# Kernel optimization log

Measured on AMD Instinct MI355X. Metric: run time of the kernel, lower is better.

## Reference

```python
import jax, jax.numpy as jnp
import numpy as np

D = 512      # n_embd
H = 8        # n_head
L = 2        # n_layer (per stack)
T = 2048     # sequence length / block_size
B = 1        # batch
BANDS = (999, 9)  # band_width for [phase, tool] stacks
EPS = 1e-5


def _sinusoidal(n_pos, dim):
    pos = np.arange(n_pos)[:, None].astype(np.float64)
    j = np.arange(dim)[None, :]
    angle = pos / np.power(10000.0, 2 * (j // 2) / dim)
    out = np.zeros((n_pos, dim), np.float32)
    out[:, 0::2] = np.sin(angle[:, 0::2])
    out[:, 1::2] = np.cos(angle[:, 1::2])
    return jnp.asarray(out)


def setup_inputs() -> dict:
    key = jax.random.key(0)
    ks = jax.random.split(key, 8)
    s = 0.02
    rn = lambda k, shp: jax.random.normal(k, shp, jnp.float32) * s
    inp = {
        "x": jax.random.normal(ks[0], (B, T, D), jnp.float32),
        "pos_emb": _sinusoidal(T, D),            # sinusoidal, frozen
        # leading dim 2 = [phase stack, tool stack], then layer dim L
        "ln1_w": jnp.ones((2, L, D)), "ln1_b": jnp.zeros((2, L, D)),
        "ln2_w": jnp.ones((2, L, D)), "ln2_b": jnp.zeros((2, L, D)),
        "Wq": rn(ks[1], (2, L, D, D)), "bq": jnp.zeros((2, L, D)),
        "Wk": rn(ks[2], (2, L, D, D)), "bk": jnp.zeros((2, L, D)),
        "Wv": rn(ks[3], (2, L, D, D)), "bv": jnp.zeros((2, L, D)),
        "Wo": rn(ks[4], (2, L, D, D)), "bo": jnp.zeros((2, L, D)),
        "W1": rn(ks[5], (2, L, D, 2 * D)), "b1": jnp.zeros((2, L, 2 * D)),
        "W2": rn(ks[6], (2, L, 2 * D, D)), "b2": jnp.zeros((2, L, D)),
        "lnf_w": jnp.ones((D,)), "lnf_b": jnp.zeros((D,)),
    }
    return inp


def _ln(x, w, b):
    mu = x.mean(-1, keepdims=True)
    var = ((x - mu) ** 2).mean(-1, keepdims=True)
    return (x - mu) / jnp.sqrt(var + EPS) * w + b


def _attn(x, Wq, bq, Wk, bk, Wv, bv, Wo, bo, bw):
    Bx, Tx, _ = x.shape
    Dh = D // H
    heads = lambda W, b: (x @ W + b).reshape(Bx, Tx, H, Dh).transpose(0, 2, 1, 3)
    q, k, v = heads(Wq, bq), heads(Wk, bk), heads(Wv, bv)
    att = jnp.einsum('bhqd,bhkd->bhqk', q, k) / jnp.sqrt(jnp.float32(Dh))
    i = jnp.arange(Tx)[:, None]
    j = jnp.arange(Tx)[None, :]
    mask = (j <= i) & (j >= i - bw)  # causal band
    att = jnp.where(mask, att, -jnp.inf)
    att = jax.nn.softmax(att, axis=-1)
    y = jnp.einsum('bhqk,bhkd->bhqd', att, v).transpose(0, 2, 1, 3).reshape(Bx, Tx, D)
    return y @ Wo + bo


def reference(x, pos_emb, ln1_w, ln1_b, ln2_w, ln2_b,
              Wq, bq, Wk, bk, Wv, bv, Wo, bo,
              W1, b1, W2, b2, lnf_w, lnf_b):
    Tx = x.shape[1]
    h0 = x + pos_emb[None, :Tx]
    outs = []
    for s in range(2):  # phase stack, tool stack
        bw = BANDS[s]
        h = h0
        for l in range(L):
            h = h + _attn(_ln(h, ln1_w[s, l], ln1_b[s, l]),
                          Wq[s, l], bq[s, l], Wk[s, l], bk[s, l],
                          Wv[s, l], bv[s, l], Wo[s, l], bo[s, l], bw)
            hm = _ln(h, ln2_w[s, l], ln2_b[s, l])
            h = h + (jax.nn.gelu(hm @ W1[s, l] + b1[s, l], approximate=False)
                     @ W2[s, l] + b2[s, l])
        outs.append(_ln(h, lnf_w, lnf_b))
    return (outs[0], outs[1])
```

## Files before the change

### kernel.cpp

```cpp
#include <hip/hip_runtime.h>
#include <stdint.h>

#define T 2048
#define D 512
#define NH 8
#define DH 64
#define L 2

typedef float floatx4 __attribute__((ext_vector_type(4)));
typedef short shortx8 __attribute__((ext_vector_type(8)));
typedef unsigned short u16;
typedef unsigned short u16x4 __attribute__((ext_vector_type(4)));

__device__ __forceinline__ u16 f2bf(float f) {
    union { float f; uint32_t u; } c; c.f = f;
    uint32_t u = c.u;
    u += 0x7fffu + ((u >> 16) & 1u);
    return (u16)(u >> 16);
}

__device__ __forceinline__ float bf2f(u16 v) {
    union { uint32_t u; float f; } c; c.u = ((uint32_t)v) << 16;
    return c.f;
}

__device__ __forceinline__ void load_lds16(const void* g, void* l) {
    __builtin_amdgcn_global_load_lds((const __attribute__((address_space(1))) void*)g,
                                     (__attribute__((address_space(3))) void*)l,
                                     16, 0, 0);
}

struct TransJobs {
    const float* src[6];
    u16* dst[6];
    const float* x;
    const float* pos;
    float* h;
};

__global__ __launch_bounds__(256) void pre_kernel(TransJobs j) {
    __shared__ float tile[32][33];
    int tid = threadIdx.x;
    if (blockIdx.z == 24) {
        int idx = (blockIdx.y * 32 + blockIdx.x) * 256 + tid;
        float4 xv = ((const float4*)j.x)[idx];
        float4 pv = ((const float4*)j.pos)[idx];
        float4 r;
        r.x = xv.x + pv.x; r.y = xv.y + pv.y; r.z = xv.z + pv.z; r.w = xv.w + pv.w;
        ((float4*)j.h)[idx] = r;
        ((float4*)j.h)[idx + (T * D / 4)] = r;
        return;
    }
    int m = blockIdx.z >> 2, slice = blockIdx.z & 3;
    int R = (m == 5) ? 1024 : 512;
    int C = (m == 4) ? 1024 : 512;
    if (blockIdx.x * 32 >= C || blockIdx.y * 32 >= R) return;
    const float* in = j.src[m] + (size_t)slice * R * C;
    u16* out = j.dst[m] + (size_t)slice * R * C;
    int tx = tid & 31, ty = tid >> 5;
    int x = blockIdx.x * 32 + tx;
    int y0 = blockIdx.y * 32;
#pragma unroll
    for (int i = 0; i < 4; i++)
        tile[ty + i * 8][tx] = in[(size_t)(y0 + ty + i * 8) * C + x];
    __syncthreads();
    int ox = y0 + tx;
#pragma unroll
    for (int i = 0; i < 4; i++)
        out[(size_t)(blockIdx.x * 32 + ty + i * 8) * R + ox] = f2bf(tile[tx][ty + i * 8]);
}

__global__ __launch_bounds__(256) void ln_res_kernel(float* __restrict__ h,
                                                     const u16* __restrict__ part,
                                                     const float* __restrict__ w0,
                                                     const float* __restrict__ b0,
                                                     u16* __restrict__ out, int l) {
    int row = blockIdx.x * 4 + (threadIdx.x >> 6);
    int lane = threadIdx.x & 63;
    int s = row >> 11;
    int c0 = lane * 4;
    float* xr = h + (size_t)row * D;
    float4 v0 = *(const float4*)(xr + c0);
    float4 v1 = *(const float4*)(xr + c0 + 256);
    if (part) {
        const u16* p0r = part + (size_t)s * 2 * T * D + (size_t)(row & (T - 1)) * D;
        const u16* p1r = p0r + (size_t)T * D;
        u16x4 a0 = *(const u16x4*)(p0r + c0), a1 = *(const u16x4*)(p0r + c0 + 256);
        u16x4 e0 = *(const u16x4*)(p1r + c0), e1 = *(const u16x4*)(p1r + c0 + 256);
        v0.x += bf2f(a0[0]) + bf2f(e0[0]); v0.y += bf2f(a0[1]) + bf2f(e0[1]);
        v0.z += bf2f(a0[2]) + bf2f(e0[2]); v0.w += bf2f(a0[3]) + bf2f(e0[3]);
        v1.x += bf2f(a1[0]) + bf2f(e1[0]); v1.y += bf2f(a1[1]) + bf2f(e1[1]);
        v1.z += bf2f(a1[2]) + bf2f(e1[2]); v1.w += bf2f(a1[3]) + bf2f(e1[3]);
        *(float4*)(xr + c0) = v0;
        *(float4*)(xr + c0 + 256) = v1;
    }
    float sum = v0.x + v0.y + v0.z + v0.w + v1.x + v1.y + v1.z + v1.w;
    float sq = v0.x*v0.x + v0.y*v0.y + v0.z*v0.z + v0.w*v0.w
             + v1.x*v1.x + v1.y*v1.y + v1.z*v1.z + v1.w*v1.w;
#pragma unroll
    for (int d2 = 1; d2 < 64; d2 <<= 1) { sum += __shfl_xor(sum, d2); sq += __shfl_xor(sq, d2); }
    float mu = sum * (1.0f / D);
    float var = sq * (1.0f / D) - mu * mu;
    float rstd = rsqrtf(var + 1e-5f);
    const float* w = w0 + (size_t)(s * L + l) * D;
    const float* b = b0 + (size_t)(s * L + l) * D;
    u16x4 p0, p1;
#pragma unroll
    for (int jj = 0; jj < 4; jj++) {
        float a = (jj == 0 ? v0.x : jj == 1 ? v0.y : jj == 2 ? v0.z : v0.w);
        p0[jj] = f2bf((a - mu) * rstd * w[c0 + jj] + b[c0 + jj]);
        float c = (jj == 0 ? v1.x : jj == 1 ? v1.y : jj == 2 ? v1.z : v1.w);
        p1[jj] = f2bf((c - mu) * rstd * w[c0 + 256 + jj] + b[c0 + 256 + jj]);
    }
    *(u16x4*)(out + (size_t)row * D + c0) = p0;
    *(u16x4*)(out + (size_t)row * D + c0 + 256) = p1;
}

__global__ __launch_bounds__(256) void lnf_kernel(const float* __restrict__ h,
                                                  const u16* __restrict__ part,
                                                  const float* __restrict__ w,
                                                  const float* __restrict__ b,
                                                  float* __restrict__ out) {
    int row = blockIdx.x * 4 + (threadIdx.x >> 6);
    int lane = threadIdx.x & 63;
    int s = row >> 11;
    int c0 = lane * 4;
    const float* xr = h + (size_t)row * D;
    float4 v0 = *(const float4*)(xr + c0);
    float4 v1 = *(const float4*)(xr + c0 + 256);
    const u16* p0r = part + (size_t)s * 2 * T * D + (size_t)(row & (T - 1)) * D;
    const u16* p1r = p0r + (size_t)T * D;
    u16x4 a0 = *(const u16x4*)(p0r + c0), a1 = *(const u16x4*)(p0r + c0 + 256);
    u16x4 e0 = *(const u16x4*)(p1r + c0), e1 = *(const u16x4*)(p1r + c0 + 256);
    v0.x += bf2f(a0[0]) + bf2f(e0[0]); v0.y += bf2f(a0[1]) + bf2f(e0[1]);
    v0.z += bf2f(a0[2]) + bf2f(e0[2]); v0.w += bf2f(a0[3]) + bf2f(e0[3]);
    v1.x += bf2f(a1[0]) + bf2f(e1[0]); v1.y += bf2f(a1[1]) + bf2f(e1[1]);
    v1.z += bf2f(a1[2]) + bf2f(e1[2]); v1.w += bf2f(a1[3]) + bf2f(e1[3]);
    float sum = v0.x + v0.y + v0.z + v0.w + v1.x + v1.y + v1.z + v1.w;
    float sq = v0.x*v0.x + v0.y*v0.y + v0.z*v0.z + v0.w*v0.w
             + v1.x*v1.x + v1.y*v1.y + v1.z*v1.z + v1.w*v1.w;
#pragma unroll
    for (int d2 = 1; d2 < 64; d2 <<= 1) { sum += __shfl_xor(sum, d2); sq += __shfl_xor(sq, d2); }
    float mu = sum * (1.0f / D);
    float var = sq * (1.0f / D) - mu * mu;
    float rstd = rsqrtf(var + 1e-5f);
    float4 r0, r1;
    r0.x = (v0.x - mu) * rstd * w[c0+0] + b[c0+0];
    r0.y = (v0.y - mu) * rstd * w[c0+1] + b[c0+1];
    r0.z = (v0.z - mu) * rstd * w[c0+2] + b[c0+2];
    r0.w = (v0.w - mu) * rstd * w[c0+3] + b[c0+3];
    r1.x = (v1.x - mu) * rstd * w[c0+256+0] + b[c0+256+0];
    r1.y = (v1.y - mu) * rstd * w[c0+256+1] + b[c0+256+1];
    r1.z = (v1.z - mu) * rstd * w[c0+256+2] + b[c0+256+2];
    r1.w = (v1.w - mu) * rstd * w[c0+256+3] + b[c0+256+3];
    *(float4*)(out + (size_t)row * D + c0) = r0;
    *(float4*)(out + (size_t)row * D + c0 + 256) = r1;
}

struct GemmPtrs {
    const u16* A[6];
    const u16* Bt[6];
    const float* bias[6];
    void* C[6];
};

#define EPI_QKV  0
#define EPI_GELU 1
#define EPI_PART 2

template <int EPI>
__global__ __launch_bounds__(256) void gemm_kernel(GemmPtrs p, int M, int N, int K, int KS) {
    __shared__ __align__(16) u16 lA[2][64 * 32];
    __shared__ __align__(16) u16 lB[2][64 * 32];
    int nchunk = K / KS;
    int pidx = blockIdx.z / nchunk;
    int kc = blockIdx.z % nchunk;
    int koff = kc * KS;
    const u16* A = p.A[pidx];
    const u16* Bt = p.Bt[pidx];
    int m0 = blockIdx.y * 64, n0 = blockIdx.x * 64;
    int tid = threadIdx.x;
    int lane = tid & 63, wave = tid >> 6;
    int wx = wave & 1, wy = wave >> 1;
    int l16 = lane & 15, q4 = lane >> 4;
    const u16* ag = A + (size_t)(m0 + (tid >> 2)) * K + koff + (tid & 3) * 8;
    const u16* bg = Bt + (size_t)(n0 + (tid >> 2)) * K + koff + (tid & 3) * 8;
    floatx4 acc[2][2] = {};
    for (int k0 = 0; k0 < KS; k0 += 64) {
        __syncthreads();
#pragma unroll
        for (int kh = 0; kh < 2; kh++) {
            load_lds16(ag + k0 + kh * 32, &lA[kh][tid * 8]);
            load_lds16(bg + k0 + kh * 32, &lB[kh][tid * 8]);
        }
        __syncthreads();
#pragma unroll
        for (int kh = 0; kh < 2; kh++) {
            shortx8 af[2], bf[2];
#pragma unroll
            for (int t = 0; t < 2; t++) {
                af[t] = *(const shortx8*)(&lA[kh][(wy * 32 + t * 16 + l16) * 32 + q4 * 8]);
                bf[t] = *(const shortx8*)(&lB[kh][(wx * 32 + t * 16 + l16) * 32 + q4 * 8]);
            }
#pragma unroll
            for (int i = 0; i < 2; i++)
#pragma unroll
                for (int j = 0; j < 2; j++)
                    acc[i][j] = __builtin_amdgcn_mfma_f32_16x16x32_bf16(af[i], bf[j], acc[i][j], 0, 0, 0);
        }
    }
    const float* bias = p.bias[pidx];
    bool vtrans = (EPI == EPI_QKV) && (pidx % 3 == 2);
#pragma unroll
    for (int i = 0; i < 2; i++) {
        int row0 = m0 + wy * 32 + i * 16 + q4 * 4;
#pragma unroll
        for (int j = 0; j < 2; j++) {
            int col = n0 + wx * 32 + j * 16 + l16;
            float bz = (kc == 0) ? bias[col] : 0.0f;
            floatx4 a = acc[i][j];
            if (EPI == EPI_QKV) {
                if (vtrans) {
                    u16x4 pk;
#pragma unroll
                    for (int r = 0; r < 4; r++) pk[r] = f2bf(a[r] + bz);
                    *(u16x4*)((u16*)p.C[pidx] + (size_t)col * M + row0) = pk;
                } else {
#pragma unroll
                    for (int r = 0; r < 4; r++)
                        ((u16*)p.C[pidx])[(size_t)(row0 + r) * N + col] = f2bf(a[r] + bz);
                }
            } else if (EPI == EPI_GELU) {
#pragma unroll
                for (int r = 0; r < 4; r++) {
                    float v = a[r] + bz;
                    float g = 0.5f * v * (1.0f + erff(v * 0.70710678118f));
                    ((u16*)p.C[pidx])[(size_t)(row0 + r) * N + col] = f2bf(g);
                }
            } else {
#pragma unroll
                for (int r = 0; r < 4; r++)
                    ((u16*)p.C[pidx])[(size_t)kc * M * N + (size_t)(row0 + r) * N + col] = f2bf(a[r] + bz);
            }
        }
    }
}

__global__ __launch_bounds__(256) void attn_kernel(const u16* __restrict__ qg,
                                                   const u16* __restrict__ kg,
                                                   const u16* __restrict__ vtg,
                                                   u16* __restrict__ ao,
                                                   int bw0, int bw1) {
    __shared__ __align__(16) u16 pbuf[4][16 * 32];
    __shared__ float cl[4][16];
    __shared__ float co[4][16][64];
    int s = blockIdx.z, hh = blockIdx.y, q0 = blockIdx.x * 16;
    int bw = (s == 0) ? bw0 : bw1;
    int tid = threadIdx.x, wave = tid >> 6, lane = tid & 63;
    int l16 = lane & 15, q4 = lane >> 4;
    const u16* Q = qg + (size_t)s * T * D;
    const u16* Kp = kg + (size_t)s * T * D;
    const u16* V = vtg + (size_t)s * D * T;
    int hd = hh * DH;
    shortx8 qf0 = *(const shortx8*)(Q + (size_t)(q0 + l16) * D + hd + q4 * 8);
    shortx8 qf1 = *(const shortx8*)(Q + (size_t)(q0 + l16) * D + hd + 32 + q4 * 8);
    floatx4 o[4] = {};
    float lsum[4] = {};
    int klo = q0 - bw; if (klo < 0) klo = 0; klo &= ~31;
    int khi = q0 + 15;
    u16* pw = pbuf[wave];
    for (int kt = klo + wave * 32; kt <= khi; kt += 128) {
        floatx4 s0 = {}, s1 = {};
        {
            shortx8 kf0 = *(const shortx8*)(Kp + (size_t)(kt + l16) * D + hd + q4 * 8);
            shortx8 kf1 = *(const shortx8*)(Kp + (size_t)(kt + l16) * D + hd + 32 + q4 * 8);
            s0 = __builtin_amdgcn_mfma_f32_16x16x32_bf16(qf0, kf0, s0, 0, 0, 0);
            s0 = __builtin_amdgcn_mfma_f32_16x16x32_bf16(qf1, kf1, s0, 0, 0, 0);
            shortx8 kf2 = *(const shortx8*)(Kp + (size_t)(kt + 16 + l16) * D + hd + q4 * 8);
            shortx8 kf3 = *(const shortx8*)(Kp + (size_t)(kt + 16 + l16) * D + hd + 32 + q4 * 8);
            s1 = __builtin_amdgcn_mfma_f32_16x16x32_bf16(qf0, kf2, s1, 0, 0, 0);
            s1 = __builtin_amdgcn_mfma_f32_16x16x32_bf16(qf1, kf3, s1, 0, 0, 0);
        }
#pragma unroll
        for (int r = 0; r < 4; r++) {
            int row = q0 + q4 * 4 + r;
            int c0 = kt + l16, c1 = kt + 16 + l16;
            float p0 = (c0 <= row && c0 >= row - bw) ? __expf(s0[r] * 0.125f) : 0.0f;
            float p1 = (c1 <= row && c1 >= row - bw) ? __expf(s1[r] * 0.125f) : 0.0f;
            lsum[r] += p0 + p1;
            pw[(q4 * 4 + r) * 32 + l16] = f2bf(p0);
            pw[(q4 * 4 + r) * 32 + 16 + l16] = f2bf(p1);
        }
        shortx8 pf = *(const shortx8*)(pw + l16 * 32 + q4 * 8);
#pragma unroll
        for (int n = 0; n < 4; n++) {
            shortx8 vf = *(const shortx8*)(V + (size_t)(hd + n * 16 + l16) * T + kt + q4 * 8);
            o[n] = __builtin_amdgcn_mfma_f32_16x16x32_bf16(pf, vf, o[n], 0, 0, 0);
        }
    }
#pragma unroll
    for (int r = 0; r < 4; r++) {
#pragma unroll
        for (int d2 = 1; d2 < 16; d2 <<= 1) lsum[r] += __shfl_xor(lsum[r], d2);
    }
    if (l16 == 0) {
#pragma unroll
        for (int r = 0; r < 4; r++) cl[wave][q4 * 4 + r] = lsum[r];
    }
#pragma unroll
    for (int n = 0; n < 4; n++)
#pragma unroll
        for (int r = 0; r < 4; r++)
            co[wave][q4 * 4 + r][n * 16 + l16] = o[n][r];
    __syncthreads();
#pragma unroll
    for (int i = 0; i < 4; i++) {
        int idx = tid + i * 256;
        int row = idx >> 6, col = idx & 63;
        float Ls = cl[0][row] + cl[1][row] + cl[2][row] + cl[3][row];
        float O = co[0][row][col] + co[1][row][col] + co[2][row][col] + co[3][row][col];
        ao[(size_t)s * T * D + (size_t)(q0 + row) * D + hd + col] = f2bf(O / Ls);
    }
}

extern "C" void kernel_launch(void* const* d_in, const int* in_sizes, int n_in,
                              void* d_out, int out_size, void* d_ws, size_t ws_size,
                              hipStream_t stream) {
    (void)in_sizes; (void)n_in; (void)out_size; (void)ws_size;
    const float* x     = (const float*)d_in[0];
    const float* pos   = (const float*)d_in[1];
    const float* ln1_w = (const float*)d_in[2];
    const float* ln1_b = (const float*)d_in[3];
    const float* ln2_w = (const float*)d_in[4];
    const float* ln2_b = (const float*)d_in[5];
    const float* Wq    = (const float*)d_in[6];
    const float* bq    = (const float*)d_in[7];
    const float* Wk    = (const float*)d_in[8];
    const float* bk    = (const float*)d_in[9];
    const float* Wv    = (const float*)d_in[10];
    const float* bv    = (const float*)d_in[11];
    const float* Wo    = (const float*)d_in[12];
    const float* bo    = (const float*)d_in[13];
    const float* W1    = (const float*)d_in[14];
    const float* b1    = (const float*)d_in[15];
    const float* W2    = (const float*)d_in[16];
    const float* b2    = (const float*)d_in[17];
    const float* lnf_w = (const float*)d_in[18];
    const float* lnf_b = (const float*)d_in[19];

    char* ws = (char*)d_ws;
    size_t off = 0;
    auto alloc = [&](size_t bytes) { void* p = ws + off; off += (bytes + 255) & ~(size_t)255; return p; };
    u16* WqT = (u16*)alloc((size_t)4 * 512 * 512 * 2);
    u16* WkT = (u16*)alloc((size_t)4 * 512 * 512 * 2);
    u16* WvT = (u16*)alloc((size_t)4 * 512 * 512 * 2);
    u16* WoT = (u16*)alloc((size_t)4 * 512 * 512 * 2);
    u16* W1T = (u16*)alloc((size_t)4 * 512 * 1024 * 2);
    u16* W2T = (u16*)alloc((size_t)4 * 1024 * 512 * 2);
    float* h = (float*)alloc((size_t)2 * T * D * 4);
    u16* xln = (u16*)alloc((size_t)2 * T * D * 2);
    u16* qb  = (u16*)alloc((size_t)2 * T * D * 2);
    u16* kb  = (u16*)alloc((size_t)2 * T * D * 2);
    u16* vt  = (u16*)alloc((size_t)2 * T * D * 2);
    u16* ao  = (u16*)alloc((size_t)2 * T * D * 2);
    u16* ff  = (u16*)alloc((size_t)2 * T * 1024 * 2);
    u16* pp = (u16*)alloc((size_t)2 * 2 * T * D * 2);
    u16* pf = (u16*)alloc((size_t)2 * 2 * T * D * 2);

    TransJobs tj;
    tj.src[0] = Wq; tj.dst[0] = WqT;
    tj.src[1] = Wk; tj.dst[1] = WkT;
    tj.src[2] = Wv; tj.dst[2] = WvT;
    tj.src[3] = Wo; tj.dst[3] = WoT;
    tj.src[4] = W1; tj.dst[4] = W1T;
    tj.src[5] = W2; tj.dst[5] = W2T;
    tj.x = x; tj.pos = pos; tj.h = h;
    pre_kernel<<<dim3(32, 32, 25), 256, 0, stream>>>(tj);

    for (int l = 0; l < L; l++) {
        ln_res_kernel<<<(2 * T) / 4, 256, 0, stream>>>(h, l == 0 ? nullptr : pf,
                                                       ln1_w, ln1_b, xln, l);

        GemmPtrs g{};
        for (int s = 0; s < 2; s++) {
            int wo = s * L + l;
            const u16* a = xln + (size_t)s * T * D;
            g.A[s * 3 + 0] = a; g.Bt[s * 3 + 0] = WqT + (size_t)wo * 512 * 512;
            g.bias[s * 3 + 0] = bq + (size_t)wo * 512; g.C[s * 3 + 0] = qb + (size_t)s * T * D;
            g.A[s * 3 + 1] = a; g.Bt[s * 3 + 1] = WkT + (size_t)wo * 512 * 512;
            g.bias[s * 3 + 1] = bk + (size_t)wo * 512; g.C[s * 3 + 1] = kb + (size_t)s * T * D;
            g.A[s * 3 + 2] = a; g.Bt[s * 3 + 2] = WvT + (size_t)wo * 512 * 512;
            g.bias[s * 3 + 2] = bv + (size_t)wo * 512; g.C[s * 3 + 2] = vt + (size_t)s * T * D;
        }
        gemm_kernel<EPI_QKV><<<dim3(8, 32, 6), 256, 0, stream>>>(g, T, 512, 512, 512);

        attn_kernel<<<dim3(128, 8, 2), 256, 0, stream>>>(qb, kb, vt, ao, 999, 9);

        GemmPtrs gp{};
        for (int s = 0; s < 2; s++) {
            int wo = s * L + l;
            gp.A[s] = ao + (size_t)s * T * D;
            gp.Bt[s] = WoT + (size_t)wo * 512 * 512;
            gp.bias[s] = bo + (size_t)wo * 512;
            gp.C[s] = pp + (size_t)s * 2 * T * D;
        }
        gemm_kernel<EPI_PART><<<dim3(8, 32, 4), 256, 0, stream>>>(gp, T, 512, 512, 256);

        ln_res_kernel<<<(2 * T) / 4, 256, 0, stream>>>(h, pp, ln2_w, ln2_b, xln, l);

        GemmPtrs g1{};
        for (int s = 0; s < 2; s++) {
            int wo = s * L + l;
            g1.A[s] = xln + (size_t)s * T * D;
            g1.Bt[s] = W1T + (size_t)wo * 512 * 1024;
            g1.bias[s] = b1 + (size_t)wo * 1024;
            g1.C[s] = ff + (size_t)s * T * 1024;
        }
        gemm_kernel<EPI_GELU><<<dim3(16, 32, 2), 256, 0, stream>>>(g1, T, 1024, 512, 512);

        GemmPtrs g2{};
        for (int s = 0; s < 2; s++) {
            int wo = s * L + l;
            g2.A[s] = ff + (size_t)s * T * 1024;
            g2.Bt[s] = W2T + (size_t)wo * 1024 * 512;
            g2.bias[s] = b2 + (size_t)wo * 512;
            g2.C[s] = pf + (size_t)s * 2 * T * D;
        }
        gemm_kernel<EPI_PART><<<dim3(8, 32, 4), 256, 0, stream>>>(g2, T, 512, 1024, 512);
    }

    lnf_kernel<<<(2 * T) / 4, 256, 0, stream>>>(h, pf, lnf_w, lnf_b, (float*)d_out);
}
```

Baseline: 327.8 us.

## Store residual stream in bf16 and software-prefetch K/V tiles in attention

The fp32 residual buffer h becomes bf16, which halves its read and write traffic in the pre, layernorm-residual and final layernorm kernels. Separately, the attention inner loop now loads the next iteration's K and V fragments into registers before running softmax and the PV MFMAs, so global-load latency overlaps with compute. The bf16 residual loses precision over the layers and may move outputs further from the reference. The prefetch adds register pressure.

Measured after the change: 319.8 us, median of 2. -2.4%, faster.

```diff
diff --git a/kernel.cpp b/kernel.cpp
--- a/kernel.cpp
+++ b/kernel.cpp
@@ -35,7 +35,7 @@
     u16* dst[6];
     const float* x;
     const float* pos;
-    float* h;
+    u16* h;
 };
 
 __global__ __launch_bounds__(256) void pre_kernel(TransJobs j) {
@@ -45,10 +45,11 @@
         int idx = (blockIdx.y * 32 + blockIdx.x) * 256 + tid;
         float4 xv = ((const float4*)j.x)[idx];
         float4 pv = ((const float4*)j.pos)[idx];
-        float4 r;
-        r.x = xv.x + pv.x; r.y = xv.y + pv.y; r.z = xv.z + pv.z; r.w = xv.w + pv.w;
-        ((float4*)j.h)[idx] = r;
-        ((float4*)j.h)[idx + (T * D / 4)] = r;
+        u16x4 hh;
+        hh[0] = f2bf(xv.x + pv.x); hh[1] = f2bf(xv.y + pv.y);
+        hh[2] = f2bf(xv.z + pv.z); hh[3] = f2bf(xv.w + pv.w);
+        ((u16x4*)j.h)[idx] = hh;
+        ((u16x4*)j.h)[idx + (T * D / 4)] = hh;
         return;
     }
     int m = blockIdx.z >> 2, slice = blockIdx.z & 3;
@@ -70,18 +71,21 @@
         out[(size_t)(blockIdx.x * 32 + ty + i * 8) * R + ox] = f2bf(tile[tx][ty + i * 8]);
 }
 
-__global__ __launch_bounds__(256) void ln_res_kernel(float* __restrict__ h,
+__global__ __launch_bounds__(256) void ln_res_kernel(u16* __restrict__ h,
                                                      const u16* __restrict__ part,
-                                                     const float* __restrict__ w0,
-                                                     const float* __restrict__ b0,
+                                                     const float* __restrict__ wp,
+                                                     const float* __restrict__ bp,
                                                      u16* __restrict__ out, int l) {
     int row = blockIdx.x * 4 + (threadIdx.x >> 6);
     int lane = threadIdx.x & 63;
     int s = row >> 11;
     int c0 = lane * 4;
-    float* xr = h + (size_t)row * D;
-    float4 v0 = *(const float4*)(xr + c0);
-    float4 v1 = *(const float4*)(xr + c0 + 256);
+    u16* xr = h + (size_t)row * D;
+    u16x4 h0 = *(const u16x4*)(xr + c0);
+    u16x4 h1 = *(const u16x4*)(xr + c0 + 256);
+    float4 v0, v1;
+    v0.x = bf2f(h0[0]); v0.y = bf2f(h0[1]); v0.z = bf2f(h0[2]); v0.w = bf2f(h0[3]);
+    v1.x = bf2f(h1[0]); v1.y = bf2f(h1[1]); v1.z = bf2f(h1[2]); v1.w = bf2f(h1[3]);
     if (part) {
         const u16* p0r = part + (size_t)s * 2 * T * D + (size_t)(row & (T - 1)) * D;
         const u16* p1r = p0r + (size_t)T * D;
@@ -91,8 +95,11 @@
         v0.z += bf2f(a0[2]) + bf2f(e0[2]); v0.w += bf2f(a0[3]) + bf2f(e0[3]);
         v1.x += bf2f(a1[0]) + bf2f(e1[0]); v1.y += bf2f(a1[1]) + bf2f(e1[1]);
         v1.z += bf2f(a1[2]) + bf2f(e1[2]); v1.w += bf2f(a1[3]) + bf2f(e1[3]);
-        *(float4*)(xr + c0) = v0;
-        *(float4*)(xr + c0 + 256) = v1;
+        u16x4 s0, s1;
+        s0[0] = f2bf(v0.x); s0[1] = f2bf(v0.y); s0[2] = f2bf(v0.z); s0[3] = f2bf(v0.w);
+        s1[0] = f2bf(v1.x); s1[1] = f2bf(v1.y); s1[2] = f2bf(v1.z); s1[3] = f2bf(v1.w);
+        *(u16x4*)(xr + c0) = s0;
+        *(u16x4*)(xr + c0 + 256) = s1;
     }
     float sum = v0.x + v0.y + v0.z + v0.w + v1.x + v1.y + v1.z + v1.w;
     float sq = v0.x*v0.x + v0.y*v0.y + v0.z*v0.z + v0.w*v0.w
@@ -102,8 +109,8 @@
     float mu = sum * (1.0f / D);
     float var = sq * (1.0f / D) - mu * mu;
     float rstd = rsqrtf(var + 1e-5f);
-    const float* w = w0 + (size_t)(s * L + l) * D;
-    const float* b = b0 + (size_t)(s * L + l) * D;
+    const float* w = wp + (size_t)(s * L + l) * D;
+    const float* b = bp + (size_t)(s * L + l) * D;
     u16x4 p0, p1;
 #pragma unroll
     for (int jj = 0; jj < 4; jj++) {
@@ -116,7 +123,7 @@
     *(u16x4*)(out + (size_t)row * D + c0 + 256) = p1;
 }
 
-__global__ __launch_bounds__(256) void lnf_kernel(const float* __restrict__ h,
+__global__ __launch_bounds__(256) void lnf_kernel(const u16* __restrict__ h,
                                                   const u16* __restrict__ part,
                                                   const float* __restrict__ w,
                                                   const float* __restrict__ b,
@@ -125,9 +132,12 @@
     int lane = threadIdx.x & 63;
     int s = row >> 11;
     int c0 = lane * 4;
-    const float* xr = h + (size_t)row * D;
-    float4 v0 = *(const float4*)(xr + c0);
-    float4 v1 = *(const float4*)(xr + c0 + 256);
+    const u16* xr = h + (size_t)row * D;
+    u16x4 h0 = *(const u16x4*)(xr + c0);
+    u16x4 h1 = *(const u16x4*)(xr + c0 + 256);
+    float4 v0, v1;
+    v0.x = bf2f(h0[0]); v0.y = bf2f(h0[1]); v0.z = bf2f(h0[2]); v0.w = bf2f(h0[3]);
+    v1.x = bf2f(h1[0]); v1.y = bf2f(h1[1]); v1.z = bf2f(h1[2]); v1.w = bf2f(h1[3]);
     const u16* p0r = part + (size_t)s * 2 * T * D + (size_t)(row & (T - 1)) * D;
     const u16* p1r = p0r + (size_t)T * D;
     u16x4 a0 = *(const u16x4*)(p0r + c0), a1 = *(const u16x4*)(p0r + c0 + 256);
@@ -269,17 +279,35 @@
     int klo = q0 - bw; if (klo < 0) klo = 0; klo &= ~31;
     int khi = q0 + 15;
     u16* pw = pbuf[wave];
-    for (int kt = klo + wave * 32; kt <= khi; kt += 128) {
+    int kt0 = klo + wave * 32;
+    shortx8 kf0, kf1, kf2, kf3, vf0, vf1, vf2, vf3;
+    if (kt0 <= khi) {
+        kf0 = *(const shortx8*)(Kp + (size_t)(kt0 + l16) * D + hd + q4 * 8);
+        kf1 = *(const shortx8*)(Kp + (size_t)(kt0 + l16) * D + hd + 32 + q4 * 8);
+        kf2 = *(const shortx8*)(Kp + (size_t)(kt0 + 16 + l16) * D + hd + q4 * 8);
+        kf3 = *(const shortx8*)(Kp + (size_t)(kt0 + 16 + l16) * D + hd + 32 + q4 * 8);
+        vf0 = *(const shortx8*)(V + (size_t)(hd + 0 * 16 + l16) * T + kt0 + q4 * 8);
+        vf1 = *(const shortx8*)(V + (size_t)(hd + 1 * 16 + l16) * T + kt0 + q4 * 8);
+        vf2 = *(const shortx8*)(V + (size_t)(hd + 2 * 16 + l16) * T + kt0 + q4 * 8);
+        vf3 = *(const shortx8*)(V + (size_t)(hd + 3 * 16 + l16) * T + kt0 + q4 * 8);
+    }
+    for (int kt = kt0; kt <= khi; kt += 128) {
         floatx4 s0 = {}, s1 = {};
-        {
-            shortx8 kf0 = *(const shortx8*)(Kp + (size_t)(kt + l16) * D + hd + q4 * 8);
-            shortx8 kf1 = *(const shortx8*)(Kp + (size_t)(kt + l16) * D + hd + 32 + q4 * 8);
-            s0 = __builtin_amdgcn_mfma_f32_16x16x32_bf16(qf0, kf0, s0, 0, 0, 0);
-            s0 = __builtin_amdgcn_mfma_f32_16x16x32_bf16(qf1, kf1, s0, 0, 0, 0);
-            shortx8 kf2 = *(const shortx8*)(Kp + (size_t)(kt + 16 + l16) * D + hd + q4 * 8);
-            shortx8 kf3 = *(const shortx8*)(Kp + (size_t)(kt + 16 + l16) * D + hd + 32 + q4 * 8);
-            s1 = __builtin_amdgcn_mfma_f32_16x16x32_bf16(qf0, kf2, s1, 0, 0, 0);
-            s1 = __builtin_amdgcn_mfma_f32_16x16x32_bf16(qf1, kf3, s1, 0, 0, 0);
+        s0 = __builtin_amdgcn_mfma_f32_16x16x32_bf16(qf0, kf0, s0, 0, 0, 0);
+        s0 = __builtin_amdgcn_mfma_f32_16x16x32_bf16(qf1, kf1, s0, 0, 0, 0);
+        s1 = __builtin_amdgcn_mfma_f32_16x16x32_bf16(qf0, kf2, s1, 0, 0, 0);
+        s1 = __builtin_amdgcn_mfma_f32_16x16x32_bf16(qf1, kf3, s1, 0, 0, 0);
+        int ktn = kt + 128;
+        shortx8 nk0, nk1, nk2, nk3, nv0, nv1, nv2, nv3;
+        if (ktn <= khi) {
+            nk0 = *(const shortx8*)(Kp + (size_t)(ktn + l16) * D + hd + q4 * 8);
+            nk1 = *(const shortx8*)(Kp + (size_t)(ktn + l16) * D + hd + 32 + q4 * 8);
+            nk2 = *(const shortx8*)(Kp + (size_t)(ktn + 16 + l16) * D + hd + q4 * 8);
+            nk3 = *(const shortx8*)(Kp + (size_t)(ktn + 16 + l16) * D + hd + 32 + q4 * 8);
+            nv0 = *(const shortx8*)(V + (size_t)(hd + 0 * 16 + l16) * T + ktn + q4 * 8);
+            nv1 = *(const shortx8*)(V + (size_t)(hd + 1 * 16 + l16) * T + ktn + q4 * 8);
+            nv2 = *(const shortx8*)(V + (size_t)(hd + 2 * 16 + l16) * T + ktn + q4 * 8);
+            nv3 = *(const shortx8*)(V + (size_t)(hd + 3 * 16 + l16) * T + ktn + q4 * 8);
         }
 #pragma unroll
         for (int r = 0; r < 4; r++) {
@@ -292,11 +320,12 @@
             pw[(q4 * 4 + r) * 32 + 16 + l16] = f2bf(p1);
         }
         shortx8 pf = *(const shortx8*)(pw + l16 * 32 + q4 * 8);
-#pragma unroll
-        for (int n = 0; n < 4; n++) {
-            shortx8 vf = *(const shortx8*)(V + (size_t)(hd + n * 16 + l16) * T + kt + q4 * 8);
-            o[n] = __builtin_amdgcn_mfma_f32_16x16x32_bf16(pf, vf, o[n], 0, 0, 0);
-        }
+        o[0] = __builtin_amdgcn_mfma_f32_16x16x32_bf16(pf, vf0, o[0], 0, 0, 0);
+        o[1] = __builtin_amdgcn_mfma_f32_16x16x32_bf16(pf, vf1, o[1], 0, 0, 0);
+        o[2] = __builtin_amdgcn_mfma_f32_16x16x32_bf16(pf, vf2, o[2], 0, 0, 0);
+        o[3] = __builtin_amdgcn_mfma_f32_16x16x32_bf16(pf, vf3, o[3], 0, 0, 0);
+        kf0 = nk0; kf1 = nk1; kf2 = nk2; kf3 = nk3;
+        vf0 = nv0; vf1 = nv1; vf2 = nv2; vf3 = nv3;
     }
 #pragma unroll
     for (int r = 0; r < 4; r++) {
@@ -357,7 +386,7 @@
     u16* WoT = (u16*)alloc((size_t)4 * 512 * 512 * 2);
     u16* W1T = (u16*)alloc((size_t)4 * 512 * 1024 * 2);
     u16* W2T = (u16*)alloc((size_t)4 * 1024 * 512 * 2);
-    float* h = (float*)alloc((size_t)2 * T * D * 4);
+    u16* h   = (u16*)alloc((size_t)2 * T * D * 2);
     u16* xln = (u16*)alloc((size_t)2 * T * D * 2);
     u16* qb  = (u16*)alloc((size_t)2 * T * D * 2);
     u16* kb  = (u16*)alloc((size_t)2 * T * D * 2);
```
